# Performance work log

Measured on AMD Instinct MI355X. Metric: run time of the kernel, lower is better.

## Reference

```python
import jax, jax.numpy as jnp
import numpy as np

D_MODEL = 1024


def setup_inputs() -> dict:
    key = jax.random.key(0)
    ks = jax.random.split(key, 11)
    B, Sq, Skv, D = 16, 2048, 2048, D_MODEL
    s = 1.0 / np.sqrt(D)
    return {
        "q": jax.random.normal(ks[0], (B, Sq, D), jnp.float32),
        "k": jax.random.normal(ks[1], (B, Skv, D), jnp.float32),
        "v": jax.random.normal(ks[2], (B, Skv, D), jnp.float32),
        "Wq": jax.random.normal(ks[3], (D, D), jnp.float32) * s,
        "bq": jnp.zeros((D,), jnp.float32),
        "Wk": jax.random.normal(ks[4], (D, D), jnp.float32) * s,
        "bk": jnp.zeros((D,), jnp.float32),
        "Wv": jax.random.normal(ks[5], (D, D), jnp.float32) * s,
        "bv": jnp.zeros((D,), jnp.float32),
        "Wo": jax.random.normal(ks[6], (D, D), jnp.float32) * s,
        "bo": jnp.zeros((D,), jnp.float32),
    }


def reference(q, k, v, Wq, bq, Wk, bk, Wv, bv, Wo, bo):
    D = q.shape[-1]
    # Projections (torch Linear: x @ W^T + b; here W stored as [in, out])
    query = q @ Wq + bq          # [B, Sq, D]
    key_p = k @ Wk + bk          # [B, Skv, D]
    value = v @ Wv + bv          # [B, Skv, D]
    # Scaled dot-product attention, scale by sqrt(d_model) (single head)
    scores = jnp.einsum('bqd,bkd->bqk', query / jnp.sqrt(jnp.float32(D)), key_p)
    attn = jax.nn.softmax(scores, axis=-1)   # dropout p=0.0 -> identity
    out = jnp.einsum('bqk,bkd->bqd', attn, value)
    return out @ Wo + bo
```

## Files before the change

kernel.cpp:

```cpp
#include <hip/hip_runtime.h>

typedef unsigned int u32;
typedef unsigned short u16;
typedef __attribute__((ext_vector_type(8))) __bf16 bf16x8;
typedef __attribute__((ext_vector_type(4))) float f32x4;

typedef __attribute__((address_space(1))) void as1_void;
typedef __attribute__((address_space(3))) void as3_void;

__device__ __forceinline__ u16 f2bf(float f){
  u32 u = __builtin_bit_cast(u32, f);
  return (u16)((u + 0x7FFFu + ((u >> 16) & 1u)) >> 16);
}
__device__ __forceinline__ float bf2f(u16 h){
  u32 u = ((u32)h) << 16;
  return __builtin_bit_cast(float, u);
}

__device__ __forceinline__ void gload16(const void* g, void* l){
  __builtin_amdgcn_global_load_lds((as1_void*)(unsigned long long)g, (as3_void*)l, 16, 0, 0);
}
__device__ __forceinline__ bf16x8 ldfrag(const char* p){
  return __builtin_bit_cast(bf16x8, *(const uint4*)p);
}

__global__ void wcast(const float* __restrict__ W, float scale, u16* __restrict__ out){
  __shared__ float t[32][33];
  int bx = blockIdx.x * 32, by = blockIdx.y * 32;
  int tx = threadIdx.x, ty = threadIdx.y;
  #pragma unroll
  for (int i = 0; i < 32; i += 8) t[ty + i][tx] = W[(size_t)(bx + ty + i) * 1024 + by + tx];
  __syncthreads();
  #pragma unroll
  for (int i = 0; i < 32; i += 8)
    out[(size_t)(by + ty + i) * 1024 + bx + tx] = f2bf(scale * t[tx][ty + i]);
}

__global__ __launch_bounds__(256) void castbf(const float* __restrict__ in, u16* __restrict__ out, int n8){
  int stride = gridDim.x * blockDim.x;
  for (int i = blockIdx.x * blockDim.x + threadIdx.x; i < n8; i += stride){
    const float4* p = (const float4*)(in + (size_t)i * 8);
    float4 f0 = p[0], f1 = p[1];
    union { uint4 u; u16 h[8]; } uu;
    uu.h[0]=f2bf(f0.x); uu.h[1]=f2bf(f0.y); uu.h[2]=f2bf(f0.z); uu.h[3]=f2bf(f0.w);
    uu.h[4]=f2bf(f1.x); uu.h[5]=f2bf(f1.y); uu.h[6]=f2bf(f1.z); uu.h[7]=f2bf(f1.w);
    ((uint4*)out)[i] = uu.u;
  }
}

__global__ __launch_bounds__(256) void softmax_rows(u16* __restrict__ S){
  __shared__ float red[8];
  size_t row = blockIdx.x;
  uint4* p = (uint4*)(S + row * 2048);
  int tid = threadIdx.x;
  int lane = tid & 63, wave = tid >> 6;
  union { uint4 u4; u16 h[8]; } uu;
  uu.u4 = p[tid];
  float v[8];
  float m = -1e30f;
  #pragma unroll
  for (int j = 0; j < 8; j++){ v[j] = bf2f(uu.h[j]); m = fmaxf(m, v[j]); }
  #pragma unroll
  for (int o = 32; o; o >>= 1) m = fmaxf(m, __shfl_xor(m, o));
  if (lane == 0) red[wave] = m;
  __syncthreads();
  m = fmaxf(fmaxf(red[0], red[1]), fmaxf(red[2], red[3]));
  float s = 0.f;
  #pragma unroll
  for (int j = 0; j < 8; j++){ v[j] = __expf(v[j] - m); s += v[j]; }
  #pragma unroll
  for (int o = 32; o; o >>= 1) s += __shfl_xor(s, o);
  if (lane == 0) red[4 + wave] = s;
  __syncthreads();
  s = red[4] + red[5] + red[6] + red[7];
  float inv = 1.f / s;
  #pragma unroll
  for (int j = 0; j < 8; j++) uu.h[j] = f2bf(v[j] * inv);
  p[tid] = uu.u4;
}


template<int MO, int N0>
__device__ __forceinline__ void phase_mfma(f32x4 (&acc)[8][4], bf16x8 (&a)[4][2], bf16x8 (&b)[4][2]){
  __builtin_amdgcn_s_setprio(1);
  #pragma unroll
  for (int ks = 0; ks < 2; ks++)
    #pragma unroll
    for (int mm = 0; mm < 4; mm++)
      #pragma unroll
      for (int nn = 0; nn < 2; nn++)
        acc[MO + mm][N0 + nn] = __builtin_amdgcn_mfma_f32_16x16x32_bf16(
            a[mm][ks], b[N0 + nn][ks], acc[MO + mm][N0 + nn], 0, 0, 0);
  __builtin_amdgcn_s_setprio(0);
}

template<int BIAS, int OUTF32>
__global__ __launch_bounds__(512, 2) void gemm8(
    const u16* __restrict__ A, const u16* __restrict__ B, void* __restrict__ C,
    const float* __restrict__ bias, float bscale, int NT,
    long long sA, long long sB, long long sC,
    int lda, int ldb, int ldc, int gx, int gxy, int TPB)
{
  __shared__ u16 sm[2][2][16384];
  char* smb = (char*)sm;

  int tid = threadIdx.x;
  int lane = tid & 63, wave = tid >> 6;
  int wr = wave >> 2, wc = wave & 3;
  int l15 = lane & 15, l4 = lane >> 4;

  int b = blockIdx.x;
  int lin0 = ((b & 7) * 32 + (b >> 3)) * TPB;

  int r = tid >> 3, cl = tid & 7;
  int ldsb = r * 128 + cl * 16;
  u32 aoff[4], boff[4];
  #pragma unroll
  for (int i = 0; i < 4; i++){
    int row = i * 64 + r;
    int ksw = (cl ^ (r & 7)) * 8;
    aoff[i] = (u32)(((u32)row * (u32)lda + (u32)ksw) * 2u);
    boff[i] = (u32)(((u32)row * (u32)ldb + (u32)ksw) * 2u);
  }
  u32 ardo[2], brdo[2];
  #pragma unroll
  for (int ks = 0; ks < 2; ks++){
    u32 sw = (u32)(((ks * 4 + l4) ^ (l15 & 7)) * 16);
    ardo[ks] = (u32)(wr * 16384 + l15 * 128) + sw;
    brdo[ks] = (u32)(wc * 8192 + l15 * 128) + sw;
  }

  auto tcoord = [&](int lin, int& x, int& y, int& z){
    z = lin / gxy; int rem = lin - z * gxy; y = rem / gx; x = rem - y * gx;
  };
  auto abase = [&](int lin){ int x, y, z; tcoord(lin, x, y, z);
    return (const char*)(A + (long long)z * sA + (size_t)(x * 256) * lda); };
  auto bbase = [&](int lin){ int x, y, z; tcoord(lin, x, y, z);
    return (const char*)(B + (long long)z * sB + (size_t)(y * 256) * ldb); };

  int tx, ty, tz;
  tcoord(lin0, tx, ty, tz);
  int row0 = tx * 256, col0 = ty * 256;
  long long zbC = tz;

  float bc0[4], bc1[4];
  if (BIAS){
    int xx, yy, zz;
    tcoord(lin0, xx, yy, zz);
    int c0 = yy * 256 + wc * 64 + l15;
    #pragma unroll
    for (int n = 0; n < 4; n++) bc0[n] = bscale * bias[c0 + n * 16];
    tcoord(lin0 + (TPB > 1 ? 1 : 0), xx, yy, zz);
    c0 = yy * 256 + wc * 64 + l15;
    #pragma unroll
    for (int n = 0; n < 4; n++) bc1[n] = bscale * bias[c0 + n * 16];
  }

  const char* AgM = abase(lin0);
  const char* AgP = AgM;
  const char* BgP = bbase(lin0);
  int km = 1, kp = 2, jm = 0, jp = 0, kk = 0, jj = 0;

#define STA(bse, i, kq, bb) gload16((bse) + aoff[i] + (size_t)(kq) * 128, smb + (bb) * 65536 + (i) * 8192 + ldsb)
#define STB(bse, i, kq, bb) gload16((bse) + boff[i] + (size_t)(kq) * 128, smb + (bb) * 65536 + 32768 + (i) * 8192 + ldsb)

  STA(AgM, 0, 0, 0); STA(AgM, 2, 0, 0);
  STB(BgP, 0, 0, 0); STB(BgP, 1, 0, 0); STB(BgP, 2, 0, 0); STB(BgP, 3, 0, 0);
  STA(AgM, 1, 0, 0); STA(AgM, 3, 0, 0);
  STA(AgM, 0, 1, 1); STA(AgM, 2, 1, 1);
  STB(BgP, 0, 1, 1); STB(BgP, 1, 1, 1); STB(BgP, 2, 1, 1); STB(BgP, 3, 1, 1);
  asm volatile("s_waitcnt vmcnt(6)" ::: "memory");
  __builtin_amdgcn_s_barrier();

  f32x4 acc[8][4] = {};
  bf16x8 a[4][2], bfr[4][2];
  int S = TPB * NT;

  for (int s = 0; s < S; s++){
    int cur = s & 1;
    const char* Ab = smb + cur * 65536;
    const char* Bb = Ab + 32768;
    bool st1 = (s + 1 < S), st2 = (s + 2 < S);

    #pragma unroll
    for (int mm = 0; mm < 4; mm++)
      #pragma unroll
      for (int ks = 0; ks < 2; ks++)
        a[mm][ks] = ldfrag(Ab + mm * 2048 + ardo[ks]);
    #pragma unroll
    for (int nn = 0; nn < 2; nn++)
      #pragma unroll
      for (int ks = 0; ks < 2; ks++)
        bfr[nn][ks] = ldfrag(Bb + nn * 2048 + brdo[ks]);
    if (st1){ STA(AgM, 1, km, cur ^ 1); STA(AgM, 3, km, cur ^ 1); }
    __builtin_amdgcn_s_barrier();
    phase_mfma<0, 0>(acc, a, bfr);
    __builtin_amdgcn_s_barrier();

    #pragma unroll
    for (int nn = 2; nn < 4; nn++)
      #pragma unroll
      for (int ks = 0; ks < 2; ks++)
        bfr[nn][ks] = ldfrag(Bb + nn * 2048 + brdo[ks]);
    if (st2){ STA(AgP, 0, kp, cur); STA(AgP, 2, kp, cur); }
    __builtin_amdgcn_s_barrier();
    phase_mfma<0, 2>(acc, a, bfr);
    __builtin_amdgcn_s_barrier();

    #pragma unroll
    for (int mm = 0; mm < 4; mm++)
      #pragma unroll
      for (int ks = 0; ks < 2; ks++)
        a[mm][ks] = ldfrag(Ab + (4 + mm) * 2048 + ardo[ks]);
    if (st2){ STB(BgP, 0, kp, cur); STB(BgP, 1, kp, cur); }
    __builtin_amdgcn_s_barrier();
    phase_mfma<4, 0>(acc, a, bfr);
    __builtin_amdgcn_s_barrier();

    if (st2){ STB(BgP, 2, kp, cur); STB(BgP, 3, kp, cur); }
    if (s < S - 2) asm volatile("s_waitcnt vmcnt(6)" ::: "memory");
    else           asm volatile("s_waitcnt vmcnt(0)" ::: "memory");
    __builtin_amdgcn_s_barrier();
    phase_mfma<4, 2>(acc, a, bfr);
    __builtin_amdgcn_s_barrier();

    if (++km == NT){ km = 0; if (++jm < TPB) AgM = abase(lin0 + jm); }
    if (++kp == NT){ kp = 0; if (++jp < TPB){ AgP = abase(lin0 + jp); BgP = bbase(lin0 + jp); } }
    if (++kk == NT){
      kk = 0;
      #pragma unroll
      for (int m = 0; m < 8; m++){
        #pragma unroll
        for (int n = 0; n < 4; n++){
          int gr0 = row0 + wr * 128 + m * 16 + l4 * 4;
          int gc  = col0 + wc * 64 + n * 16 + l15;
          float bcol = BIAS ? (jj == 0 ? bc0[n] : bc1[n]) : 0.f;
          #pragma unroll
          for (int j = 0; j < 4; j++){
            float vv = acc[m][n][j] + bcol;
            int gr = gr0 + j;
            if (OUTF32) ((float*)C)[zbC * sC + (size_t)gr * ldc + gc] = vv;
            else        ((u16*) C)[zbC * sC + (size_t)gr * ldc + gc] = f2bf(vv);
          }
          acc[m][n] = (f32x4){0.f, 0.f, 0.f, 0.f};
        }
      }
      if (++jj < TPB){
        tcoord(lin0 + jj, tx, ty, tz);
        row0 = tx * 256; col0 = ty * 256; zbC = tz;
      }
    }
  }
#undef STA
#undef STB
}

extern "C" void kernel_launch(void* const* d_in, const int* in_sizes, int n_in,
                              void* d_out, int out_size, void* d_ws, size_t ws_size,
                              hipStream_t stream){
  const float* q  = (const float*)d_in[0];
  const float* k  = (const float*)d_in[1];
  const float* v  = (const float*)d_in[2];
  const float* Wq = (const float*)d_in[3];
  const float* bq = (const float*)d_in[4];
  const float* Wk = (const float*)d_in[5];
  const float* bk = (const float*)d_in[6];
  const float* Wv = (const float*)d_in[7];
  const float* bv = (const float*)d_in[8];
  const float* Wo = (const float*)d_in[9];
  const float* bo = (const float*)d_in[10];

  char* ws = (char*)d_ws;
  const size_t MB = (size_t)1 << 20;
  u16* Wqt = (u16*)(ws + 0 * MB);
  u16* Wkt = (u16*)(ws + 2 * MB);
  u16* Wvt = (u16*)(ws + 4 * MB);
  u16* Wot = (u16*)(ws + 6 * MB);
  u16* Qp  = (u16*)(ws + 8 * MB);
  u16* Kp  = (u16*)(ws + 72 * MB);
  u16* Vt  = (u16*)(ws + 136 * MB);
  u16* S   = (u16*)(ws + 200 * MB);
  u16* O   = (u16*)(ws + 328 * MB);
  u16* X   = (u16*)(ws + 200 * MB);
  float* out = (float*)d_out;

  dim3 wb(32, 8);
  wcast<<<dim3(32, 32), wb, 0, stream>>>(Wq, 1.f / 32.f, Wqt);
  wcast<<<dim3(32, 32), wb, 0, stream>>>(Wk, 1.f, Wkt);
  wcast<<<dim3(32, 32), wb, 0, stream>>>(Wv, 1.f, Wvt);
  wcast<<<dim3(32, 32), wb, 0, stream>>>(Wo, 1.f, Wot);

  const int n8 = 16 * 2048 * 1024 / 8;

  castbf<<<dim3(2048), 256, 0, stream>>>(q, X, n8);
  gemm8<1,0><<<dim3(256), 512, 0, stream>>>(X, Wqt, Qp, bq, 1.f/32.f,
      16, 0, 0, 0, 1024, 1024, 1024, 128, 512, 2);
  castbf<<<dim3(2048), 256, 0, stream>>>(k, X, n8);
  gemm8<1,0><<<dim3(256), 512, 0, stream>>>(X, Wkt, Kp, bk, 1.f,
      16, 0, 0, 0, 1024, 1024, 1024, 128, 512, 2);
  castbf<<<dim3(2048), 256, 0, stream>>>(v, X, n8);
  gemm8<0,0><<<dim3(256), 512, 0, stream>>>(Wvt, X, Vt, nullptr, 0.f,
      16, 0, 2048LL * 1024, 1024LL * 2048, 1024, 1024, 2048, 4, 32, 2);
  gemm8<0,0><<<dim3(256), 512, 0, stream>>>(Qp, Kp, S, nullptr, 0.f,
      16, 2048LL * 1024, 2048LL * 1024, 2048LL * 2048, 1024, 1024, 2048, 8, 64, 4);
  softmax_rows<<<dim3(32768), 256, 0, stream>>>(S);
  gemm8<1,0><<<dim3(256), 512, 0, stream>>>(S, Vt, O, bv, 1.f,
      32, 2048LL * 2048, 1024LL * 2048, 2048LL * 1024, 2048, 2048, 1024, 8, 32, 2);
  gemm8<1,1><<<dim3(256), 512, 0, stream>>>(O, Wot, out, bo, 1.f,
      16, 0, 0, 0, 1024, 1024, 1024, 128, 512, 2);
}
```

Baseline: 728.2 us.

## Replace 256x256 double-buffered GEMM with 256x128 triple-buffered pipeline

Result: slower. 841.3 us (+15.5%).

```diff
diff --git a/kernel.cpp b/kernel.cpp
--- a/kernel.cpp
+++ b/kernel.cpp
@@ -80,33 +80,18 @@
 }
 
 
-template<int MO, int N0>
-__device__ __forceinline__ void phase_mfma(f32x4 (&acc)[8][4], bf16x8 (&a)[4][2], bf16x8 (&b)[4][2]){
-  __builtin_amdgcn_s_setprio(1);
-  #pragma unroll
-  for (int ks = 0; ks < 2; ks++)
-    #pragma unroll
-    for (int mm = 0; mm < 4; mm++)
-      #pragma unroll
-      for (int nn = 0; nn < 2; nn++)
-        acc[MO + mm][N0 + nn] = __builtin_amdgcn_mfma_f32_16x16x32_bf16(
-            a[mm][ks], b[N0 + nn][ks], acc[MO + mm][N0 + nn], 0, 0, 0);
-  __builtin_amdgcn_s_setprio(0);
-}
-
 template<int BIAS, int OUTF32>
-__global__ __launch_bounds__(512, 2) void gemm8(
+__global__ __launch_bounds__(512, 2) void gemmP(
     const u16* __restrict__ A, const u16* __restrict__ B, void* __restrict__ C,
     const float* __restrict__ bias, float bscale, int NT,
     long long sA, long long sB, long long sC,
     int lda, int ldb, int ldc, int gx, int gxy, int TPB)
 {
-  __shared__ u16 sm[2][2][16384];
-  char* smb = (char*)sm;
+  __shared__ __align__(16) char smb[3][49152];
 
   int tid = threadIdx.x;
   int lane = tid & 63, wave = tid >> 6;
-  int wr = wave >> 2, wc = wave & 3;
+  int wr = wave >> 1, wc = wave & 1;
   int l15 = lane & 15, l4 = lane >> 4;
 
   int b = blockIdx.x;
@@ -114,20 +99,19 @@
 
   int r = tid >> 3, cl = tid & 7;
   int ldsb = r * 128 + cl * 16;
-  u32 aoff[4], boff[4];
-  #pragma unroll
-  for (int i = 0; i < 4; i++){
-    int row = i * 64 + r;
-    int ksw = (cl ^ (r & 7)) * 8;
-    aoff[i] = (u32)(((u32)row * (u32)lda + (u32)ksw) * 2u);
-    boff[i] = (u32)(((u32)row * (u32)ldb + (u32)ksw) * 2u);
-  }
+  int ksw = (cl ^ (r & 7)) * 16;
+  u32 aoff[4], boff[2];
+  #pragma unroll
+  for (int i = 0; i < 4; i++) aoff[i] = (u32)((i * 64 + r) * lda * 2) + (u32)ksw;
+  #pragma unroll
+  for (int i = 0; i < 2; i++) boff[i] = (u32)((i * 64 + r) * ldb * 2) + (u32)ksw;
+
   u32 ardo[2], brdo[2];
   #pragma unroll
   for (int ks = 0; ks < 2; ks++){
     u32 sw = (u32)(((ks * 4 + l4) ^ (l15 & 7)) * 16);
-    ardo[ks] = (u32)(wr * 16384 + l15 * 128) + sw;
-    brdo[ks] = (u32)(wc * 8192 + l15 * 128) + sw;
+    ardo[ks] = (u32)((wr * 64 + l15) * 128) + sw;
+    brdo[ks] = (u32)(32768 + (wc * 64 + l15) * 128) + sw;
   }
 
   auto tcoord = [&](int lin, int& x, int& y, int& z){
@@ -136,123 +120,113 @@
   auto abase = [&](int lin){ int x, y, z; tcoord(lin, x, y, z);
     return (const char*)(A + (long long)z * sA + (size_t)(x * 256) * lda); };
   auto bbase = [&](int lin){ int x, y, z; tcoord(lin, x, y, z);
-    return (const char*)(B + (long long)z * sB + (size_t)(y * 256) * ldb); };
+    return (const char*)(B + (long long)z * sB + (size_t)(y * 128) * ldb); };
 
   int tx, ty, tz;
   tcoord(lin0, tx, ty, tz);
-  int row0 = tx * 256, col0 = ty * 256;
+  int row0 = tx * 256, col0 = ty * 128;
   long long zbC = tz;
 
-  float bc0[4], bc1[4];
+  float bc0[4], bc1[4], bc2[4], bc3[4];
   if (BIAS){
     int xx, yy, zz;
-    tcoord(lin0, xx, yy, zz);
-    int c0 = yy * 256 + wc * 64 + l15;
-    #pragma unroll
-    for (int n = 0; n < 4; n++) bc0[n] = bscale * bias[c0 + n * 16];
-    tcoord(lin0 + (TPB > 1 ? 1 : 0), xx, yy, zz);
-    c0 = yy * 256 + wc * 64 + l15;
-    #pragma unroll
-    for (int n = 0; n < 4; n++) bc1[n] = bscale * bias[c0 + n * 16];
-  }
-
-  const char* AgM = abase(lin0);
-  const char* AgP = AgM;
+    #pragma unroll
+    for (int jt = 0; jt < 4; jt++){
+      int lt = lin0 + (jt < TPB ? jt : 0);
+      tcoord(lt, xx, yy, zz);
+      int c0 = yy * 128 + wc * 64 + l15;
+      float* dst = jt == 0 ? bc0 : jt == 1 ? bc1 : jt == 2 ? bc2 : bc3;
+      #pragma unroll
+      for (int n = 0; n < 4; n++) dst[n] = bscale * bias[c0 + n * 16];
+    }
+  }
+
+  const char* AgP = abase(lin0);
   const char* BgP = bbase(lin0);
-  int km = 1, kp = 2, jm = 0, jp = 0, kk = 0, jj = 0;
-
-#define STA(bse, i, kq, bb) gload16((bse) + aoff[i] + (size_t)(kq) * 128, smb + (bb) * 65536 + (i) * 8192 + ldsb)
-#define STB(bse, i, kq, bb) gload16((bse) + boff[i] + (size_t)(kq) * 128, smb + (bb) * 65536 + 32768 + (i) * 8192 + ldsb)
-
-  STA(AgM, 0, 0, 0); STA(AgM, 2, 0, 0);
-  STB(BgP, 0, 0, 0); STB(BgP, 1, 0, 0); STB(BgP, 2, 0, 0); STB(BgP, 3, 0, 0);
-  STA(AgM, 1, 0, 0); STA(AgM, 3, 0, 0);
-  STA(AgM, 0, 1, 1); STA(AgM, 2, 1, 1);
-  STB(BgP, 0, 1, 1); STB(BgP, 1, 1, 1); STB(BgP, 2, 1, 1); STB(BgP, 3, 1, 1);
+  int kp = 2, jp = 0;
+
+#define STAGE6(kq, bufp) do { \
+    gload16(AgP + aoff[0] + (u32)(kq) * 128u, (bufp) + 0 * 8192 + ldsb); \
+    gload16(AgP + aoff[1] + (u32)(kq) * 128u, (bufp) + 1 * 8192 + ldsb); \
+    gload16(AgP + aoff[2] + (u32)(kq) * 128u, (bufp) + 2 * 8192 + ldsb); \
+    gload16(AgP + aoff[3] + (u32)(kq) * 128u, (bufp) + 3 * 8192 + ldsb); \
+    gload16(BgP + boff[0] + (u32)(kq) * 128u, (bufp) + 32768 + ldsb); \
+    gload16(BgP + boff[1] + (u32)(kq) * 128u, (bufp) + 40960 + ldsb); } while (0)
+
+  STAGE6(0, &smb[0][0]);
+  STAGE6(1, &smb[1][0]);
   asm volatile("s_waitcnt vmcnt(6)" ::: "memory");
   __builtin_amdgcn_s_barrier();
-
-  f32x4 acc[8][4] = {};
-  bf16x8 a[4][2], bfr[4][2];
-  int S = TPB * NT;
+  __builtin_amdgcn_sched_barrier(0);
+
+  f32x4 acc[4][4] = {};
+  int rbuf = 0, sbuf = 2;
+  int kk = 0, jj = 0;
+  int S = NT * TPB;
 
   for (int s = 0; s < S; s++){
-    int cur = s & 1;
-    const char* Ab = smb + cur * 65536;
-    const char* Bb = Ab + 32768;
-    bool st1 = (s + 1 < S), st2 = (s + 2 < S);
-
-    #pragma unroll
-    for (int mm = 0; mm < 4; mm++)
+    bool st = (s + 2 < S);
+    if (st){
+      STAGE6(kp, &smb[sbuf][0]);
+      if (++kp == NT){ kp = 0; if (++jp < TPB){ AgP = abase(lin0 + jp); BgP = bbase(lin0 + jp); } }
+    }
+
+    const char* RB = &smb[rbuf][0];
+    bf16x8 fa[4][2], fb[4][2];
+    #pragma unroll
+    for (int m = 0; m < 4; m++)
       #pragma unroll
       for (int ks = 0; ks < 2; ks++)
-        a[mm][ks] = ldfrag(Ab + mm * 2048 + ardo[ks]);
-    #pragma unroll
-    for (int nn = 0; nn < 2; nn++)
+        fa[m][ks] = ldfrag(RB + m * 2048 + ardo[ks]);
+    #pragma unroll
+    for (int n = 0; n < 4; n++)
       #pragma unroll
       for (int ks = 0; ks < 2; ks++)
-        bfr[nn][ks] = ldfrag(Bb + nn * 2048 + brdo[ks]);
-    if (st1){ STA(AgM, 1, km, cur ^ 1); STA(AgM, 3, km, cur ^ 1); }
-    __builtin_amdgcn_s_barrier();
-    phase_mfma<0, 0>(acc, a, bfr);
-    __builtin_amdgcn_s_barrier();
-
-    #pragma unroll
-    for (int nn = 2; nn < 4; nn++)
-      #pragma unroll
-      for (int ks = 0; ks < 2; ks++)
-        bfr[nn][ks] = ldfrag(Bb + nn * 2048 + brdo[ks]);
-    if (st2){ STA(AgP, 0, kp, cur); STA(AgP, 2, kp, cur); }
-    __builtin_amdgcn_s_barrier();
-    phase_mfma<0, 2>(acc, a, bfr);
-    __builtin_amdgcn_s_barrier();
-
-    #pragma unroll
-    for (int mm = 0; mm < 4; mm++)
-      #pragma unroll
-      for (int ks = 0; ks < 2; ks++)
-        a[mm][ks] = ldfrag(Ab + (4 + mm) * 2048 + ardo[ks]);
-    if (st2){ STB(BgP, 0, kp, cur); STB(BgP, 1, kp, cur); }
-    __builtin_amdgcn_s_barrier();
-    phase_mfma<4, 0>(acc, a, bfr);
-    __builtin_amdgcn_s_barrier();
-
-    if (st2){ STB(BgP, 2, kp, cur); STB(BgP, 3, kp, cur); }
-    if (s < S - 2) asm volatile("s_waitcnt vmcnt(6)" ::: "memory");
-    else           asm volatile("s_waitcnt vmcnt(0)" ::: "memory");
-    __builtin_amdgcn_s_barrier();
-    phase_mfma<4, 2>(acc, a, bfr);
-    __builtin_amdgcn_s_barrier();
-
-    if (++km == NT){ km = 0; if (++jm < TPB) AgM = abase(lin0 + jm); }
-    if (++kp == NT){ kp = 0; if (++jp < TPB){ AgP = abase(lin0 + jp); BgP = bbase(lin0 + jp); } }
+        fb[n][ks] = ldfrag(RB + n * 2048 + brdo[ks]);
+
+    __builtin_amdgcn_s_setprio(1);
+    #pragma unroll
+    for (int m = 0; m < 4; m++)
+      #pragma unroll
+      for (int n = 0; n < 4; n++)
+        #pragma unroll
+        for (int ks = 0; ks < 2; ks++)
+          acc[m][n] = __builtin_amdgcn_mfma_f32_16x16x32_bf16(fa[m][ks], fb[n][ks], acc[m][n], 0, 0, 0);
+    __builtin_amdgcn_s_setprio(0);
+
     if (++kk == NT){
       kk = 0;
       #pragma unroll
-      for (int m = 0; m < 8; m++){
+      for (int m = 0; m < 4; m++){
         #pragma unroll
         for (int n = 0; n < 4; n++){
-          int gr0 = row0 + wr * 128 + m * 16 + l4 * 4;
+          int gr0 = row0 + wr * 64 + m * 16 + l4 * 4;
           int gc  = col0 + wc * 64 + n * 16 + l15;
-          float bcol = BIAS ? (jj == 0 ? bc0[n] : bc1[n]) : 0.f;
+          float bcol = BIAS ? (jj == 0 ? bc0[n] : jj == 1 ? bc1[n] : jj == 2 ? bc2[n] : bc3[n]) : 0.f;
           #pragma unroll
           for (int j = 0; j < 4; j++){
             float vv = acc[m][n][j] + bcol;
-            int gr = gr0 + j;
-            if (OUTF32) ((float*)C)[zbC * sC + (size_t)gr * ldc + gc] = vv;
-            else        ((u16*) C)[zbC * sC + (size_t)gr * ldc + gc] = f2bf(vv);
+            if (OUTF32) ((float*)C)[zbC * sC + (size_t)(gr0 + j) * ldc + gc] = vv;
+            else        ((u16*) C)[zbC * sC + (size_t)(gr0 + j) * ldc + gc] = f2bf(vv);
           }
           acc[m][n] = (f32x4){0.f, 0.f, 0.f, 0.f};
         }
       }
       if (++jj < TPB){
         tcoord(lin0 + jj, tx, ty, tz);
-        row0 = tx * 256; col0 = ty * 256; zbC = tz;
+        row0 = tx * 256; col0 = ty * 128; zbC = tz;
       }
     }
-  }
-#undef STA
-#undef STB
+
+    if (st) asm volatile("s_waitcnt vmcnt(6)" ::: "memory");
+    else    asm volatile("s_waitcnt vmcnt(0)" ::: "memory");
+    __builtin_amdgcn_s_barrier();
+    __builtin_amdgcn_sched_barrier(0);
+
+    rbuf = rbuf == 2 ? 0 : rbuf + 1;
+    sbuf = sbuf == 2 ? 0 : sbuf + 1;
+  }
+#undef STAGE6
 }
 
 extern "C" void kernel_launch(void* const* d_in, const int* in_sizes, int n_in,
@@ -293,19 +267,19 @@
   const int n8 = 16 * 2048 * 1024 / 8;
 
   castbf<<<dim3(2048), 256, 0, stream>>>(q, X, n8);
-  gemm8<1,0><<<dim3(256), 512, 0, stream>>>(X, Wqt, Qp, bq, 1.f/32.f,
-      16, 0, 0, 0, 1024, 1024, 1024, 128, 512, 2);
+  gemmP<1,0><<<dim3(256), 512, 0, stream>>>(X, Wqt, Qp, bq, 1.f/32.f,
+      16, 0, 0, 0, 1024, 1024, 1024, 128, 1024, 4);
   castbf<<<dim3(2048), 256, 0, stream>>>(k, X, n8);
-  gemm8<1,0><<<dim3(256), 512, 0, stream>>>(X, Wkt, Kp, bk, 1.f,
-      16, 0, 0, 0, 1024, 1024, 1024, 128, 512, 2);
+  gemmP<1,0><<<dim3(256), 512, 0, stream>>>(X, Wkt, Kp, bk, 1.f,
+      16, 0, 0, 0, 1024, 1024, 1024, 128, 1024, 4);
   castbf<<<dim3(2048), 256, 0, stream>>>(v, X, n8);
-  gemm8<0,0><<<dim3(256), 512, 0, stream>>>(Wvt, X, Vt, nullptr, 0.f,
-      16, 0, 2048LL * 1024, 1024LL * 2048, 1024, 1024, 2048, 4, 32, 2);
-  gemm8<0,0><<<dim3(256), 512, 0, stream>>>(Qp, Kp, S, nullptr, 0.f,
-      16, 2048LL * 1024, 2048LL * 1024, 2048LL * 2048, 1024, 1024, 2048, 8, 64, 4);
+  gemmP<0,0><<<dim3(256), 512, 0, stream>>>(Wvt, X, Vt, nullptr, 0.f,
+      16, 0, 2048LL * 1024, 1024LL * 2048, 1024, 1024, 2048, 4, 64, 4);
+  gemmP<0,0><<<dim3(256), 512, 0, stream>>>(Qp, Kp, S, nullptr, 0.f,
+      16, 2048LL * 1024, 2048LL * 1024, 2048LL * 2048, 1024, 1024, 2048, 8, 128, 8);
   softmax_rows<<<dim3(32768), 256, 0, stream>>>(S);
-  gemm8<1,0><<<dim3(256), 512, 0, stream>>>(S, Vt, O, bv, 1.f,
-      32, 2048LL * 2048, 1024LL * 2048, 2048LL * 1024, 2048, 2048, 1024, 8, 32, 2);
-  gemm8<1,1><<<dim3(256), 512, 0, stream>>>(O, Wot, out, bo, 1.f,
-      16, 0, 0, 0, 1024, 1024, 1024, 128, 512, 2);
-}
+  gemmP<1,0><<<dim3(256), 512, 0, stream>>>(S, Vt, O, bv, 1.f,
+      32, 2048LL * 2048, 1024LL * 2048, 2048LL * 1024, 2048, 2048, 1024, 8, 64, 4);
+  gemmP<1,1><<<dim3(256), 512, 0, stream>>>(O, Wot, out, bo, 1.f,
+      16, 0, 0, 0, 1024, 1024, 1024, 128, 1024, 4);
+}
```

## Prefetch next-stage A fragments and reorder MFMA phases in GEMM loop

Applied to the files above, without the earlier changes.

Measured after the change: 740.6 us. Within noise of the previous version (+1.7%).

```diff
diff --git a/kernel.cpp b/kernel.cpp
--- a/kernel.cpp
+++ b/kernel.cpp
@@ -81,7 +81,7 @@
 
 
 template<int MO, int N0>
-__device__ __forceinline__ void phase_mfma(f32x4 (&acc)[8][4], bf16x8 (&a)[4][2], bf16x8 (&b)[4][2]){
+__device__ __forceinline__ void pm(f32x4 (&acc)[8][4], bf16x8 (&a)[4][2], bf16x8 (&b)[2][2]){
   __builtin_amdgcn_s_setprio(1);
   #pragma unroll
   for (int ks = 0; ks < 2; ks++)
@@ -90,7 +90,7 @@
       #pragma unroll
       for (int nn = 0; nn < 2; nn++)
         acc[MO + mm][N0 + nn] = __builtin_amdgcn_mfma_f32_16x16x32_bf16(
-            a[mm][ks], b[N0 + nn][ks], acc[MO + mm][N0 + nn], 0, 0, 0);
+            a[mm][ks], b[nn][ks], acc[MO + mm][N0 + nn], 0, 0, 0);
   __builtin_amdgcn_s_setprio(0);
 }
 
@@ -173,55 +173,64 @@
   __builtin_amdgcn_s_barrier();
 
   f32x4 acc[8][4] = {};
-  bf16x8 a[4][2], bfr[4][2];
+  bf16x8 aLo[4][2], aHi[4][2], b01[2][2], b23[2][2];
   int S = TPB * NT;
+
+  #pragma unroll
+  for (int mm = 0; mm < 4; mm++)
+    #pragma unroll
+    for (int ks = 0; ks < 2; ks++)
+      aLo[mm][ks] = ldfrag(smb + mm * 2048 + ardo[ks]);
 
   for (int s = 0; s < S; s++){
     int cur = s & 1;
     const char* Ab = smb + cur * 65536;
     const char* Bb = Ab + 32768;
+    const char* AbN = smb + (cur ^ 1) * 65536;
     bool st1 = (s + 1 < S), st2 = (s + 2 < S);
 
+    if (st1){ STA(AgM, 1, km, cur ^ 1); STA(AgM, 3, km, cur ^ 1); }
+    #pragma unroll
+    for (int nn = 0; nn < 2; nn++)
+      #pragma unroll
+      for (int ks = 0; ks < 2; ks++)
+        b01[nn][ks] = ldfrag(Bb + nn * 2048 + brdo[ks]);
+    #pragma unroll
+    for (int nn = 0; nn < 2; nn++)
+      #pragma unroll
+      for (int ks = 0; ks < 2; ks++)
+        b23[nn][ks] = ldfrag(Bb + (2 + nn) * 2048 + brdo[ks]);
+    __builtin_amdgcn_s_barrier();
+    pm<0, 0>(acc, aLo, b01);
+    __builtin_amdgcn_s_barrier();
+
+    if (st2){ STA(AgP, 0, kp, cur); STA(AgP, 2, kp, cur); }
     #pragma unroll
     for (int mm = 0; mm < 4; mm++)
       #pragma unroll
       for (int ks = 0; ks < 2; ks++)
-        a[mm][ks] = ldfrag(Ab + mm * 2048 + ardo[ks]);
-    #pragma unroll
-    for (int nn = 0; nn < 2; nn++)
-      #pragma unroll
-      for (int ks = 0; ks < 2; ks++)
-        bfr[nn][ks] = ldfrag(Bb + nn * 2048 + brdo[ks]);
-    if (st1){ STA(AgM, 1, km, cur ^ 1); STA(AgM, 3, km, cur ^ 1); }
-    __builtin_amdgcn_s_barrier();
-    phase_mfma<0, 0>(acc, a, bfr);
-    __builtin_amdgcn_s_barrier();
-
-    #pragma unroll
-    for (int nn = 2; nn < 4; nn++)
-      #pragma unroll
-      for (int ks = 0; ks < 2; ks++)
-        bfr[nn][ks] = ldfrag(Bb + nn * 2048 + brdo[ks]);
-    if (st2){ STA(AgP, 0, kp, cur); STA(AgP, 2, kp, cur); }
-    __builtin_amdgcn_s_barrier();
-    phase_mfma<0, 2>(acc, a, bfr);
-    __builtin_amdgcn_s_barrier();
-
-    #pragma unroll
-    for (int mm = 0; mm < 4; mm++)
-      #pragma unroll
-      for (int ks = 0; ks < 2; ks++)
-        a[mm][ks] = ldfrag(Ab + (4 + mm) * 2048 + ardo[ks]);
+        aHi[mm][ks] = ldfrag(Ab + (4 + mm) * 2048 + ardo[ks]);
+    __builtin_amdgcn_s_barrier();
+    pm<0, 2>(acc, aLo, b23);
+    __builtin_amdgcn_s_barrier();
+
     if (st2){ STB(BgP, 0, kp, cur); STB(BgP, 1, kp, cur); }
     __builtin_amdgcn_s_barrier();
-    phase_mfma<4, 0>(acc, a, bfr);
+    pm<4, 2>(acc, aHi, b23);
     __builtin_amdgcn_s_barrier();
 
     if (st2){ STB(BgP, 2, kp, cur); STB(BgP, 3, kp, cur); }
     if (s < S - 2) asm volatile("s_waitcnt vmcnt(6)" ::: "memory");
     else           asm volatile("s_waitcnt vmcnt(0)" ::: "memory");
     __builtin_amdgcn_s_barrier();
-    phase_mfma<4, 2>(acc, a, bfr);
+    if (st1){
+      #pragma unroll
+      for (int mm = 0; mm < 4; mm++)
+        #pragma unroll
+        for (int ks = 0; ks < 2; ks++)
+          aLo[mm][ks] = ldfrag(AbN + mm * 2048 + ardo[ks]);
+    }
+    pm<4, 0>(acc, aHi, b01);
     __builtin_amdgcn_s_barrier();
 
     if (++km == NT){ km = 0; if (++jm < TPB) AgM = abase(lin0 + jm); }
```
